# Kernel tuning notes

Hardware: AMD Instinct MI355X
Metric: run time of the kernel (lower is better)

Reference implementation:

```python
import jax, jax.numpy as jnp
import numpy as np

B, N, D = 4, 4096, 256

def setup_inputs() -> dict:
    key = jax.random.key(0)
    ks = jax.random.split(key, 5)
    s = 1.0 / np.sqrt(D)
    return {
        'x': jax.random.normal(ks[0], (B, N, D), jnp.float32),
        'Wq': jax.random.normal(ks[1], (D, D), jnp.float32) * s,
        'bq': jnp.zeros((D,), jnp.float32),
        'Wk': jax.random.normal(ks[2], (D, D), jnp.float32) * s,
        'bk': jnp.zeros((D,), jnp.float32),
        'Wv': jax.random.normal(ks[3], (D, D), jnp.float32) * s,
        'bv': jnp.zeros((D,), jnp.float32),
        'Wfc': jax.random.normal(ks[4], (D, D), jnp.float32) * s,
        'bfc': jnp.zeros((D,), jnp.float32),
    }

def reference(x, Wq, bq, Wk, bk, Wv, bv, Wfc, bfc):
    # Linear layers: y = x @ W^T + b (torch nn.Linear convention)
    q = jnp.einsum('bnd,ed->bne', x, Wq) + bq
    k = jnp.einsum('bnd,ed->bne', x, Wk) + bk
    v = jnp.einsum('bnd,ed->bne', x, Wv) + bv
    # NOTE: source has no 1/sqrt(d) scaling — keep it faithful.
    attn = jnp.einsum('bnd,bmd->bnm', q, k)          # [B, N, N]
    attn = jax.nn.softmax(attn, axis=-1)
    out = jnp.einsum('bnm,bmd->bnd', attn, v)        # [B, N, D]
    out = jnp.einsum('bnd,ed->bne', out, Wfc) + bfc
    return out
```

## Files before the change

kernel.cpp:

```cpp
#include <hip/hip_runtime.h>
#include <stdint.h>

#define B_ 4
#define N_ 4096
#define D_ 256
#define M_ (B_*N_)

typedef _Float16 f16;
typedef _Float16 f16x8 __attribute__((ext_vector_type(8)));
typedef float    f32x4  __attribute__((ext_vector_type(4)));
typedef float    f32x16 __attribute__((ext_vector_type(16)));

#define MFMA16(A,B,C) __builtin_amdgcn_mfma_f32_16x16x32_f16(A,B,C,0,0,0)
#define MFMA32(A,B,C) __builtin_amdgcn_mfma_f32_32x32x16_f16(A,B,C,0,0,0)

#define QH_OFF   0u
#define KH_OFF   8388608u
#define VT_OFF   16777216u
#define WFCH_OFF 25165824u
#define WQS_OFF  25296896u
#define WKS_OFF  25559040u
#define WVS_OFF  25821184u
#define OP_OFF   26083328u
#define ML_OFF   59637760u

typedef __attribute__((address_space(3))) uint32_t lds_u32;
typedef __attribute__((address_space(1))) const uint32_t g_u32;

__device__ __forceinline__ void stage16(const f16* g, f16* lbase) {
    __builtin_amdgcn_global_load_lds((g_u32*)g, (lds_u32*)lbase, 16, 0, 0);
}
__device__ __forceinline__ uint32_t pk2(float a, float b) {
    union { f16 h[2]; uint32_t u; } x;
    x.h[0] = (f16)a; x.h[1] = (f16)b;
    return x.u;
}

__global__ __launch_bounds__(256) void cvt_w(
    const float* __restrict__ Wq, const float* __restrict__ Wk,
    const float* __restrict__ Wv, const float* __restrict__ Wfc,
    f16* __restrict__ Wqs, f16* __restrict__ Wks, f16* __restrict__ Wvs,
    f16* __restrict__ Wfch)
{
    const int z = blockIdx.y;
    const float* W = (z==0) ? Wq : (z==1) ? Wk : (z==2) ? Wv : Wfc;
    int idx = (blockIdx.x * 256 + threadIdx.x) * 4;
    float4 v = *(const float4*)(W + idx);
    union { ushort4 u4; f16 h[4]; } hi, lo;
    float vv[4] = {v.x, v.y, v.z, v.w};
    #pragma unroll
    for (int j = 0; j < 4; j++) {
        hi.h[j] = (f16)vv[j];
        lo.h[j] = (f16)(vv[j] - (float)hi.h[j]);
    }
    int col = idx >> 8, k = idx & 255;
    int dc = k >> 5, c8 = (k >> 3) & 3, j = k & 7;
    int p  = c8 ^ ((col >> 2) & 3);
    if (z == 3) {
        *(ushort4*)(Wfch + dc*8192 + col*32 + p*8 + j) = hi.u4;
    } else {
        f16* Ws = (z==0) ? Wqs : (z==1) ? Wks : Wvs;
        int base = dc*16384 + col*32 + p*8 + j;
        *(ushort4*)(Ws + base)        = hi.u4;
        *(ushort4*)(Ws + base + 8192) = lo.u4;
    }
}

__global__ __launch_bounds__(256, 2) void proj_kernel(
    const float* __restrict__ x,
    const f16* __restrict__ Wqs, const f16* __restrict__ Wks,
    const f16* __restrict__ Wvs,
    const float* __restrict__ bq, const float* __restrict__ bk,
    const float* __restrict__ bv,
    f16* __restrict__ Qh, f16* __restrict__ Kh, f16* __restrict__ Vt)
{
    const int z = blockIdx.y;
    const f16*   Ws   = (z==0) ? Wqs : (z==1) ? Wks : Wvs;
    const float* bias = (z==0) ? bq  : (z==1) ? bk  : bv;

    __shared__ __align__(16) f16 Bs[2][16384];

    const int tid  = threadIdx.x;
    const int w    = tid >> 6;
    const int lane = tid & 63;
    const int l15  = lane & 15;
    const int q4   = lane >> 4;
    const int m0   = blockIdx.x * 64 + w * 16;
    const int rowA = m0 + l15;
    const int sw   = (l15 >> 2) & 3;

    int s8[8];
    #pragma unroll
    for (int i = 0; i < 8; i++) s8[i] = (tid + i*256) * 8;

    f32x4 acc[16];
    #pragma unroll
    for (int nt = 0; nt < 16; nt++) acc[nt] = (f32x4){0.f,0.f,0.f,0.f};

    #pragma unroll
    for (int i = 0; i < 8; i++) stage16(Ws + s8[i], &Bs[0][0] + s8[i]);
    const float* xp = x + (size_t)rowA * 256;
    float4 a0 = *(const float4*)(xp + q4*8);
    float4 a1 = *(const float4*)(xp + q4*8 + 4);

    for (int dc = 0; dc < 8; dc++) {
        const int cur = dc & 1;
        __syncthreads();
        if (dc < 7) {
            const f16* src = Ws + (size_t)(dc+1)*16384;
            f16* dst = &Bs[cur ^ 1][0];
            #pragma unroll
            for (int i = 0; i < 8; i++) stage16(src + s8[i], dst + s8[i]);
        }
        float av[8] = {a0.x,a0.y,a0.z,a0.w,a1.x,a1.y,a1.z,a1.w};
        f16x8 ah, alo;
        #pragma unroll
        for (int j = 0; j < 8; j++) {
            ah[j]  = (f16)av[j];
            alo[j] = (f16)(av[j] - (float)ah[j]);
        }
        if (dc < 7) {
            a0 = *(const float4*)(xp + (dc+1)*32 + q4*8);
            a1 = *(const float4*)(xp + (dc+1)*32 + q4*8 + 4);
        }
        const f16* Bc = &Bs[cur][0];
        #pragma unroll
        for (int nt = 0; nt < 16; nt++) {
            const f16* bp = Bc + (nt*16 + l15)*32 + ((q4 ^ sw) << 3);
            f16x8 bh = *(const f16x8*)bp;
            f16x8 bl = *(const f16x8*)(bp + 8192);
            acc[nt] = MFMA16(ah,  bl, acc[nt]);
            acc[nt] = MFMA16(alo, bh, acc[nt]);
            acc[nt] = MFMA16(ah,  bh, acc[nt]);
        }
    }

    if (z == 0) {
        #pragma unroll
        for (int nt = 0; nt < 16; nt++) {
            float bb = bias[nt*16 + l15];
            #pragma unroll
            for (int r = 0; r < 4; r++)
                Qh[(size_t)(m0 + q4*4 + r)*256 + nt*16 + l15] = (f16)(acc[nt][r] + bb);
        }
    } else if (z == 1) {
        const int cbase = (l15 >> 3);
        const int j     = l15 & 7;
        #pragma unroll
        for (int nt = 0; nt < 16; nt++) {
            float bb = bias[nt*16 + l15];
            int c = nt*2 + cbase;
            #pragma unroll
            for (int r = 0; r < 4; r++) {
                int m = m0 + q4*4 + r;
                Kh[(size_t)m*256 + (size_t)((c ^ (m & 7)) << 3) + j] = (f16)(acc[nt][r] + bb);
            }
        }
    } else {
        uint32_t* VTs = (uint32_t*)&Bs[0][0];
        const int bb_ = m0 >> 12;
        const int n0  = (blockIdx.x * 64) & 4095;
        const int mloc = w*16 + q4*4;
        const int mc   = mloc >> 3;
        __syncthreads();
        #pragma unroll
        for (int nt = 0; nt < 16; nt++) {
            int e = nt*16 + l15;
            float bv_ = bias[e];
            uint32_t w0 = pk2(acc[nt][0]+bv_, acc[nt][1]+bv_);
            uint32_t w1 = pk2(acc[nt][2]+bv_, acc[nt][3]+bv_);
            int base = e*36 + ((mc ^ (e & 7)) << 2) + ((q4*2) & 3);
            VTs[base]     = w0;
            VTs[base + 1] = w1;
        }
        __syncthreads();
        #pragma unroll
        for (int i = 0; i < 8; i++) {
            int e  = w*64 + i*8 + (lane >> 3);
            int nc = lane & 7;
            const f16* src = (const f16*)&VTs[e*36 + ((nc ^ (e & 7)) << 2)];
            f16x8 v = *(const f16x8*)src;
            *(f16x8*)(Vt + ((size_t)bb_*256 + e)*4096 + n0 + nc*8) = v;
        }
    }
}

#define MARGIN 10.0f
__global__ __launch_bounds__(256, 2) void attn_kernel(
    const f16* __restrict__ Qh, const f16* __restrict__ Kh,
    const f16* __restrict__ Vt,
    f16* __restrict__ Opart, float* __restrict__ Ml)
{
    __shared__ __align__(16) f16 SMEM[32768];
    f16* Ks = SMEM;
    f16* Vs = SMEM + 16384;

    const int combo = blockIdx.x & 15;
    const int b   = combo >> 2;
    const int sp  = combo & 3;
    const int qt  = blockIdx.x >> 4;
    const int tid  = threadIdx.x;
    const int w    = tid >> 6;
    const int lane = tid & 63;
    const int l31  = lane & 31;
    const int half = lane >> 5;
    const int qbase = qt * 128 + w * 32;
    const int vx   = (l31 >> 2) & 3;

    f16x8 qf[16];
    {
        const f16* qp = Qh + ((size_t)(b*4096 + qbase + l31))*256 + half*8;
        #pragma unroll
        for (int st = 0; st < 16; st++) qf[st] = *(const f16x8*)(qp + st*16);
    }

    f32x16 Oa[8];
    #pragma unroll
    for (int t = 0; t < 8; t++)
        #pragma unroll
        for (int r = 0; r < 16; r++) Oa[t][r] = 0.f;
    float mo = -3e38f, ls = 0.f;

    const f16* kg0 = Kh + ((size_t)(b*4096 + sp*1024)) * 256;
    const f16* vg0 = Vt + ((size_t)b*256) * 4096 + sp*1024;

    int kslot[4], voff[4];
    #pragma unroll
    for (int i = 0; i < 4; i++) {
        int s = tid + i*256;
        kslot[i] = s * 8;
        int d = s >> 2;
        int kc = (s & 3) ^ ((s >> 4) & 3);
        voff[i] = d * 4096 + kc * 8;
    }

    #pragma unroll
    for (int i = 0; i < 4; i++) stage16(kg0 + kslot[i], Ks + kslot[i]);

    f16x8 bp0, bp1;

    for (int it = 0; it < 32; it++) {
        const int cur = it & 1;
        __syncthreads();
        if (it + 1 < 32) {
            const f16* kg = kg0 + (size_t)(it+1) * 8192;
            f16* kl = Ks + (cur ^ 1) * 8192;
            #pragma unroll
            for (int i = 0; i < 4; i++) stage16(kg + kslot[i], kl + kslot[i]);
        }
        {
            const f16* vg = vg0 + it*32;
            f16* vl = Vs + cur * 8192;
            #pragma unroll
            for (int i = 0; i < 4; i++) stage16(vg + voff[i], vl + kslot[i]);
        }

        const f16* krp = Ks + cur*8192 + l31*256;
        const f16* vpp = Vs + (cur^1)*8192 + l31*32;
        f32x16 sa;
        #pragma unroll
        for (int r = 0; r < 16; r++) sa[r] = 0.f;
        if (it > 0) {
            #pragma unroll
            for (int st = 0; st < 16; st++) {
                f16x8 ka = *(const f16x8*)(krp + (((st*2 + half) ^ (lane & 7)) << 3));
                sa = MFMA32(ka, qf[st], sa);
                int t = st >> 1, kh = st & 1;
                f16x8 va = *(const f16x8*)(vpp + t*1024 + (((half + kh*2) ^ vx) << 3));
                Oa[t] = MFMA32(va, kh ? bp1 : bp0, Oa[t]);
            }
        } else {
            #pragma unroll
            for (int st = 0; st < 16; st++) {
                f16x8 ka = *(const f16x8*)(krp + (((st*2 + half) ^ (lane & 7)) << 3));
                sa = MFMA32(ka, qf[st], sa);
            }
        }

        float tm = sa[0];
        #pragma unroll
        for (int r = 1; r < 16; r++) tm = fmaxf(tm, sa[r]);
        if (__any(tm > mo + MARGIN)) {
            float tmq = fmaxf(tm, __shfl_xor(tm, 32));
            float mn = fmaxf(mo, tmq);
            float al = __expf(mo - mn);
            mo = mn; ls *= al;
            #pragma unroll
            for (int t = 0; t < 8; t++)
                #pragma unroll
                for (int r = 0; r < 16; r++) Oa[t][r] *= al;
        }
        float p[16];
        #pragma unroll
        for (int r = 0; r < 16; r++) { p[r] = __expf(sa[r] - mo); ls += p[r]; }

        #pragma unroll
        for (int kh = 0; kh < 2; kh++) {
            uint32_t lo0 = pk2(p[8*kh+0], p[8*kh+1]);
            uint32_t lo1 = pk2(p[8*kh+2], p[8*kh+3]);
            uint32_t hi0 = pk2(p[8*kh+4], p[8*kh+5]);
            uint32_t hi1 = pk2(p[8*kh+6], p[8*kh+7]);
            uint32_t s0 = half ? lo0 : hi0;
            uint32_t s1 = half ? lo1 : hi1;
            uint32_t r0 = __shfl_xor(s0, 32);
            uint32_t r1 = __shfl_xor(s1, 32);
            uint32_t k0 = half ? hi0 : lo0;
            uint32_t k1 = half ? hi1 : lo1;
            union { uint32_t u[4]; f16x8 v; } bb;
            bb.u[0] = half ? r0 : k0;
            bb.u[1] = half ? r1 : k1;
            bb.u[2] = half ? k0 : r0;
            bb.u[3] = half ? k1 : r1;
            if (kh == 0) bp0 = bb.v; else bp1 = bb.v;
        }
    }

    __syncthreads();
    {
        const f16* vpp = Vs + 8192 + l31*32;
        #pragma unroll
        for (int t = 0; t < 8; t++) {
            #pragma unroll
            for (int kh = 0; kh < 2; kh++) {
                f16x8 va = *(const f16x8*)(vpp + t*1024 + (((half + kh*2) ^ vx) << 3));
                Oa[t] = MFMA32(va, kh ? bp1 : bp0, Oa[t]);
            }
        }
    }
    __syncthreads();

    float l = ls + __shfl_xor(ls, 32);
    float inv = 1.0f / l;
    f16* tb = SMEM + w * 8192;
    #pragma unroll
    for (int t = 0; t < 8; t++) {
        #pragma unroll
        for (int rp = 0; rp < 8; rp++) {
            int r0 = rp * 2;
            int d  = (r0 & 3) + 8*(r0 >> 2) + 4*half + t*32;
            int c  = d >> 3, j = d & 7;
            uint32_t wv = pk2(Oa[t][r0]*inv, Oa[t][r0+1]*inv);
            *(uint32_t*)(tb + l31*256 + ((c ^ (l31 & 7)) << 3) + (j & 6)) = wv;
        }
    }
    f16* opb = Opart + ((size_t)sp*M_ + b*4096 + qbase) * 256;
    #pragma unroll
    for (int i = 0; i < 16; i++) {
        int q = (i & 3)*8 + (lane >> 3);
        int c = (i >> 2)*8 + (lane & 7);
        f16x8 v = *(const f16x8*)(tb + q*256 + ((c ^ (q & 7)) << 3));
        *(f16x8*)(opb + (size_t)q*256 + c*8) = v;
    }
    if (half == 0) {
        size_t mrow = (size_t)sp*M_ + b*4096 + qbase + l31;
        Ml[mrow*2]     = mo;
        Ml[mrow*2 + 1] = l;
    }
}

__global__ __launch_bounds__(256, 2) void merge_fc_kernel(
    const f16* __restrict__ Opart, const float* __restrict__ Ml,
    const f16* __restrict__ Wfci, const float* __restrict__ bfc,
    float* __restrict__ out)
{
    __shared__ __align__(16) f16 Bs[2][8192];

    const int tid  = threadIdx.x;
    const int w    = tid >> 6;
    const int lane = tid & 63;
    const int l15  = lane & 15;
    const int q4   = lane >> 4;
    const int m0   = blockIdx.x * 64 + w * 16;
    const int rowA = m0 + l15;
    const int sw   = (l15 >> 2) & 3;

    int s4[4];
    #pragma unroll
    for (int i = 0; i < 4; i++) s4[i] = (tid + i*256) * 8;

    float mv[4], lv[4];
    #pragma unroll
    for (int p = 0; p < 4; p++) {
        mv[p] = Ml[((size_t)p*M_ + rowA)*2];
        lv[p] = Ml[((size_t)p*M_ + rowA)*2 + 1];
    }
    float mm = fmaxf(fmaxf(mv[0], mv[1]), fmaxf(mv[2], mv[3]));
    float cw[4], den = 0.f;
    #pragma unroll
    for (int p = 0; p < 4; p++) { cw[p] = __expf(mv[p] - mm) * lv[p]; den += cw[p]; }
    float invd = 1.0f / den;
    #pragma unroll
    for (int p = 0; p < 4; p++) cw[p] *= invd;

    #pragma unroll
    for (int i = 0; i < 4; i++) stage16(Wfci + s4[i], &Bs[0][0] + s4[i]);
    const f16* opb = Opart + (size_t)rowA*256 + q4*8;
    f16x8 of[4];
    #pragma unroll
    for (int p = 0; p < 4; p++) of[p] = *(const f16x8*)(opb + (size_t)p*M_*256);

    f32x4 acc[16];
    #pragma unroll
    for (int nt = 0; nt < 16; nt++) acc[nt] = (f32x4){0.f,0.f,0.f,0.f};

    for (int dc = 0; dc < 8; dc++) {
        const int cur = dc & 1;
        __syncthreads();
        if (dc < 7) {
            const f16* src = Wfci + (size_t)(dc+1)*8192;
            f16* dst = &Bs[cur ^ 1][0];
            #pragma unroll
            for (int i = 0; i < 4; i++) stage16(src + s4[i], dst + s4[i]);
        }
        float v[8] = {};
        #pragma unroll
        for (int p = 0; p < 4; p++)
            #pragma unroll
            for (int j = 0; j < 8; j++) v[j] += cw[p] * (float)of[p][j];
        f16x8 af;
        #pragma unroll
        for (int j = 0; j < 8; j++) af[j] = (f16)v[j];
        if (dc < 7) {
            #pragma unroll
            for (int p = 0; p < 4; p++)
                of[p] = *(const f16x8*)(opb + (size_t)p*M_*256 + (dc+1)*32);
        }
        const f16* Bc = &Bs[cur][0];
        #pragma unroll
        for (int nt = 0; nt < 16; nt++) {
            f16x8 bf = *(const f16x8*)(Bc + (nt*16 + l15)*32 + ((q4 ^ sw) << 3));
            acc[nt] = MFMA16(af, bf, acc[nt]);
        }
    }
    #pragma unroll
    for (int nt = 0; nt < 16; nt++) {
        float bias = bfc[nt*16 + l15];
        #pragma unroll
        for (int r = 0; r < 4; r++)
            out[(size_t)(m0 + q4*4 + r) * 256 + nt*16 + l15] = acc[nt][r] + bias;
    }
}

extern "C" void kernel_launch(void* const* d_in, const int* in_sizes, int n_in,
                              void* d_out, int out_size, void* d_ws, size_t ws_size,
                              hipStream_t stream)
{
    const float* x   = (const float*)d_in[0];
    const float* Wq  = (const float*)d_in[1];
    const float* bq  = (const float*)d_in[2];
    const float* Wk  = (const float*)d_in[3];
    const float* bk  = (const float*)d_in[4];
    const float* Wv  = (const float*)d_in[5];
    const float* bv  = (const float*)d_in[6];
    const float* Wfc = (const float*)d_in[7];
    const float* bfc = (const float*)d_in[8];
    float* out = (float*)d_out;

    char* ws = (char*)d_ws;
    f16*   Qh    = (f16*)(ws + QH_OFF);
    f16*   Kh    = (f16*)(ws + KH_OFF);
    f16*   Vt    = (f16*)(ws + VT_OFF);
    f16*   Wfch  = (f16*)(ws + WFCH_OFF);
    f16*   Wqs   = (f16*)(ws + WQS_OFF);
    f16*   Wks   = (f16*)(ws + WKS_OFF);
    f16*   Wvs   = (f16*)(ws + WVS_OFF);
    f16*   Opart = (f16*)(ws + OP_OFF);
    float* Ml    = (float*)(ws + ML_OFF);

    cvt_w<<<dim3(64, 4), 256, 0, stream>>>(Wq, Wk, Wv, Wfc, Wqs, Wks, Wvs, Wfch);
    proj_kernel<<<dim3(256, 3), 256, 0, stream>>>(x, Wqs, Wks, Wvs, bq, bk, bv, Qh, Kh, Vt);
    attn_kernel<<<512, 256, 0, stream>>>(Qh, Kh, Vt, Opart, Ml);
    merge_fc_kernel<<<256, 256, 0, stream>>>(Opart, Ml, Wfch, bfc, out);
}
```

Before: 207.8 us.

## Software-pipeline softmax exp with QK MFMA and fold log2e into Q

Restructures the attention loop into a two-stage pipeline. Each iteration computes the exp of the previous tile's scores while the current tile's QK MFMAs issue, then runs the PV MFMAs. The loop is unrolled by two with templated buffer indices and setprio hints. Q is prescaled by log2(e) so the kernel can use a native exp2 instead of __expf, and the combine step switches to exp2 to match. This adds register pressure from holding two score tiles, and f16 Q now carries the scale factor, which changes rounding slightly.

After: 632.3 us. 3.04x slower.

```diff
diff --git a/kernel.cpp b/kernel.cpp
--- a/kernel.cpp
+++ b/kernel.cpp
@@ -34,6 +34,13 @@
     union { f16 h[2]; uint32_t u; } x;
     x.h[0] = (f16)a; x.h[1] = (f16)b;
     return x.u;
+}
+__device__ __forceinline__ float exp2_fast(float x) {
+#if __has_builtin(__builtin_amdgcn_exp2f)
+    return __builtin_amdgcn_exp2f(x);
+#else
+    return exp2f(x);
+#endif
 }
 
 __global__ __launch_bounds__(256) void cvt_w(
@@ -141,7 +148,8 @@
             float bb = bias[nt*16 + l15];
             #pragma unroll
             for (int r = 0; r < 4; r++)
-                Qh[(size_t)(m0 + q4*4 + r)*256 + nt*16 + l15] = (f16)(acc[nt][r] + bb);
+                Qh[(size_t)(m0 + q4*4 + r)*256 + nt*16 + l15] =
+                    (f16)((acc[nt][r] + bb) * 1.44269504088896f);
         }
     } else if (z == 1) {
         const int cbase = (l15 >> 3);
@@ -185,7 +193,103 @@
     }
 }
 
-#define MARGIN 10.0f
+#define MARGIN2 12.0f
+
+__device__ __forceinline__ void build_bp(const float* p, int half,
+                                         f16x8& bp0, f16x8& bp1)
+{
+    #pragma unroll
+    for (int kh = 0; kh < 2; kh++) {
+        uint32_t lo0 = pk2(p[8*kh+0], p[8*kh+1]);
+        uint32_t lo1 = pk2(p[8*kh+2], p[8*kh+3]);
+        uint32_t hi0 = pk2(p[8*kh+4], p[8*kh+5]);
+        uint32_t hi1 = pk2(p[8*kh+6], p[8*kh+7]);
+        uint32_t s0 = half ? lo0 : hi0;
+        uint32_t s1 = half ? lo1 : hi1;
+        uint32_t r0 = __shfl_xor(s0, 32);
+        uint32_t r1 = __shfl_xor(s1, 32);
+        uint32_t k0 = half ? hi0 : lo0;
+        uint32_t k1 = half ? hi1 : lo1;
+        union { uint32_t u[4]; f16x8 v; } bb;
+        bb.u[0] = half ? r0 : k0;
+        bb.u[1] = half ? r1 : k1;
+        bb.u[2] = half ? k0 : r0;
+        bb.u[3] = half ? k1 : r1;
+        if (kh == 0) bp0 = bb.v; else bp1 = bb.v;
+    }
+}
+
+template<int CUR, bool FIRST, bool LAST>
+__device__ __forceinline__ void attn_body(
+    int it, f32x16& SA, const f32x16& SP, f32x16* Oa, const f16x8* qf,
+    f16x8& bp0, f16x8& bp1, float& mo, float& ls,
+    f16* __restrict__ Ks, f16* __restrict__ Vs,
+    const f16* __restrict__ kg0, const f16* __restrict__ vg0,
+    const int* kslot, const int* voff,
+    int l31, int half, int vx, int lane)
+{
+    __syncthreads();
+    if (!LAST) {
+        const f16* kg = kg0 + (size_t)(it+1) * 8192;
+        f16* kl = Ks + (CUR ^ 1) * 8192;
+        #pragma unroll
+        for (int i = 0; i < 4; i++) stage16(kg + kslot[i], kl + kslot[i]);
+    }
+    {
+        const f16* vg = vg0 + it*32;
+        f16* vl = Vs + CUR * 8192;
+        #pragma unroll
+        for (int i = 0; i < 4; i++) stage16(vg + voff[i], vl + kslot[i]);
+    }
+
+    const f16* krp = Ks + CUR*8192 + l31*256;
+    #pragma unroll
+    for (int r = 0; r < 16; r++) SA[r] = 0.f;
+
+    float p[16];
+    __builtin_amdgcn_s_setprio(1);
+    #pragma unroll
+    for (int st = 0; st < 16; st++) {
+        f16x8 ka = *(const f16x8*)(krp + (((st*2 + half) ^ (lane & 7)) << 3));
+        SA = MFMA32(ka, qf[st], SA);
+        if (!FIRST) p[st] = exp2_fast(SP[st] - mo);
+    }
+    if (!FIRST) {
+        float s0 = (p[0]+p[1]) + (p[2]+p[3]);
+        float s1 = (p[4]+p[5]) + (p[6]+p[7]);
+        float s2 = (p[8]+p[9]) + (p[10]+p[11]);
+        float s3 = (p[12]+p[13]) + (p[14]+p[15]);
+        ls += (s0+s1) + (s2+s3);
+        build_bp(p, half, bp0, bp1);
+        const f16* vpp = Vs + (CUR^1)*8192 + l31*32;
+        #pragma unroll
+        for (int t = 0; t < 8; t++) {
+            #pragma unroll
+            for (int kh = 0; kh < 2; kh++) {
+                f16x8 va = *(const f16x8*)(vpp + t*1024 + (((half + kh*2) ^ vx) << 3));
+                Oa[t] = MFMA32(va, kh ? bp1 : bp0, Oa[t]);
+            }
+        }
+    }
+    __builtin_amdgcn_s_setprio(0);
+
+    float t0 = fmaxf(fmaxf(SA[0],SA[1]),   fmaxf(SA[2],SA[3]));
+    float t1 = fmaxf(fmaxf(SA[4],SA[5]),   fmaxf(SA[6],SA[7]));
+    float t2 = fmaxf(fmaxf(SA[8],SA[9]),   fmaxf(SA[10],SA[11]));
+    float t3 = fmaxf(fmaxf(SA[12],SA[13]), fmaxf(SA[14],SA[15]));
+    float tm = fmaxf(fmaxf(t0,t1), fmaxf(t2,t3));
+    if (__any(tm > mo + MARGIN2)) {
+        float tmq = fmaxf(tm, __shfl_xor(tm, 32));
+        float mn = fmaxf(mo, tmq);
+        float al = exp2_fast(mo - mn);
+        mo = mn; ls *= al;
+        #pragma unroll
+        for (int t = 0; t < 8; t++)
+            #pragma unroll
+            for (int r = 0; r < 16; r++) Oa[t][r] *= al;
+    }
+}
+
 __global__ __launch_bounds__(256, 2) void attn_kernel(
     const f16* __restrict__ Qh, const f16* __restrict__ Kh,
     const f16* __restrict__ Vt,
@@ -238,85 +342,32 @@
     for (int i = 0; i < 4; i++) stage16(kg0 + kslot[i], Ks + kslot[i]);
 
     f16x8 bp0, bp1;
-
-    for (int it = 0; it < 32; it++) {
-        const int cur = it & 1;
-        __syncthreads();
-        if (it + 1 < 32) {
-            const f16* kg = kg0 + (size_t)(it+1) * 8192;
-            f16* kl = Ks + (cur ^ 1) * 8192;
-            #pragma unroll
-            for (int i = 0; i < 4; i++) stage16(kg + kslot[i], kl + kslot[i]);
-        }
-        {
-            const f16* vg = vg0 + it*32;
-            f16* vl = Vs + cur * 8192;
-            #pragma unroll
-            for (int i = 0; i < 4; i++) stage16(vg + voff[i], vl + kslot[i]);
-        }
-
-        const f16* krp = Ks + cur*8192 + l31*256;
-        const f16* vpp = Vs + (cur^1)*8192 + l31*32;
-        f32x16 sa;
-        #pragma unroll
-        for (int r = 0; r < 16; r++) sa[r] = 0.f;
-        if (it > 0) {
-            #pragma unroll
-            for (int st = 0; st < 16; st++) {
-                f16x8 ka = *(const f16x8*)(krp + (((st*2 + half) ^ (lane & 7)) << 3));
-                sa = MFMA32(ka, qf[st], sa);
-                int t = st >> 1, kh = st & 1;
-                f16x8 va = *(const f16x8*)(vpp + t*1024 + (((half + kh*2) ^ vx) << 3));
-                Oa[t] = MFMA32(va, kh ? bp1 : bp0, Oa[t]);
-            }
-        } else {
-            #pragma unroll
-            for (int st = 0; st < 16; st++) {
-                f16x8 ka = *(const f16x8*)(krp + (((st*2 + half) ^ (lane & 7)) << 3));
-                sa = MFMA32(ka, qf[st], sa);
-            }
-        }
-
-        float tm = sa[0];
-        #pragma unroll
-        for (int r = 1; r < 16; r++) tm = fmaxf(tm, sa[r]);
-        if (__any(tm > mo + MARGIN)) {
-            float tmq = fmaxf(tm, __shfl_xor(tm, 32));
-            float mn = fmaxf(mo, tmq);
-            float al = __expf(mo - mn);
-            mo = mn; ls *= al;
-            #pragma unroll
-            for (int t = 0; t < 8; t++)
-                #pragma unroll
-                for (int r = 0; r < 16; r++) Oa[t][r] *= al;
-        }
-        float p[16];
-        #pragma unroll
-        for (int r = 0; r < 16; r++) { p[r] = __expf(sa[r] - mo); ls += p[r]; }
-
-        #pragma unroll
-        for (int kh = 0; kh < 2; kh++) {
-            uint32_t lo0 = pk2(p[8*kh+0], p[8*kh+1]);
-            uint32_t lo1 = pk2(p[8*kh+2], p[8*kh+3]);
-            uint32_t hi0 = pk2(p[8*kh+4], p[8*kh+5]);
-            uint32_t hi1 = pk2(p[8*kh+6], p[8*kh+7]);
-            uint32_t s0 = half ? lo0 : hi0;
-            uint32_t s1 = half ? lo1 : hi1;
-            uint32_t r0 = __shfl_xor(s0, 32);
-            uint32_t r1 = __shfl_xor(s1, 32);
-            uint32_t k0 = half ? hi0 : lo0;
-            uint32_t k1 = half ? hi1 : lo1;
-            union { uint32_t u[4]; f16x8 v; } bb;
-            bb.u[0] = half ? r0 : k0;
-            bb.u[1] = half ? r1 : k1;
-            bb.u[2] = half ? k0 : r0;
-            bb.u[3] = half ? k1 : r1;
-            if (kh == 0) bp0 = bb.v; else bp1 = bb.v;
-        }
-    }
+    f32x16 saA, saB;
+    #pragma unroll
+    for (int r = 0; r < 16; r++) { saA[r] = 0.f; saB[r] = 0.f; }
+
+    attn_body<0, true,  false>(0, saA, saB, Oa, qf, bp0, bp1, mo, ls,
+                               Ks, Vs, kg0, vg0, kslot, voff, l31, half, vx, lane);
+    for (int itp = 0; itp < 15; itp++) {
+        attn_body<1, false, false>(2*itp+1, saB, saA, Oa, qf, bp0, bp1, mo, ls,
+                                   Ks, Vs, kg0, vg0, kslot, voff, l31, half, vx, lane);
+        attn_body<0, false, false>(2*itp+2, saA, saB, Oa, qf, bp0, bp1, mo, ls,
+                                   Ks, Vs, kg0, vg0, kslot, voff, l31, half, vx, lane);
+    }
+    attn_body<1, false, true>(31, saB, saA, Oa, qf, bp0, bp1, mo, ls,
+                              Ks, Vs, kg0, vg0, kslot, voff, l31, half, vx, lane);
 
     __syncthreads();
     {
+        float p[16];
+        #pragma unroll
+        for (int r = 0; r < 16; r++) p[r] = exp2_fast(saB[r] - mo);
+        float s0 = (p[0]+p[1]) + (p[2]+p[3]);
+        float s1 = (p[4]+p[5]) + (p[6]+p[7]);
+        float s2 = (p[8]+p[9]) + (p[10]+p[11]);
+        float s3 = (p[12]+p[13]) + (p[14]+p[15]);
+        ls += (s0+s1) + (s2+s3);
+        build_bp(p, half, bp0, bp1);
         const f16* vpp = Vs + 8192 + l31*32;
         #pragma unroll
         for (int t = 0; t < 8; t++) {
@@ -387,7 +438,7 @@
     float mm = fmaxf(fmaxf(mv[0], mv[1]), fmaxf(mv[2], mv[3]));
     float cw[4], den = 0.f;
     #pragma unroll
-    for (int p = 0; p < 4; p++) { cw[p] = __expf(mv[p] - mm) * lv[p]; den += cw[p]; }
+    for (int p = 0; p < 4; p++) { cw[p] = exp2_fast(mv[p] - mm) * lv[p]; den += cw[p]; }
     float invd = 1.0f / den;
     #pragma unroll
     for (int p = 0; p < 4; p++) cw[p] *= invd;
```

## Halve proj weight staging tiles and split merge_fc output columns across waves

Applied to the files above, without the earlier changes.

The projection kernel now stages the weight in half-width chunks (128 output columns per phase, 16 phases), which halves shared memory per block. The launch bound is raised to allow 3 blocks per CU, and the V transpose epilogue runs in two passes. The merge/FC kernel assigns two waves per 16-row tile, each computing half the output columns, and doubles the grid to 512 blocks to fill more CUs. The cost is more barriers and phases in proj, and merge_fc now re-reads the Opart partials and redoes the softmax-merge weighting twice per row.

After: 211.5 us. Within noise of the previous version (+1.8%).

```diff
diff --git a/kernel.cpp b/kernel.cpp
--- a/kernel.cpp
+++ b/kernel.cpp
@@ -60,13 +60,14 @@
         *(ushort4*)(Wfch + dc*8192 + col*32 + p*8 + j) = hi.u4;
     } else {
         f16* Ws = (z==0) ? Wqs : (z==1) ? Wks : Wvs;
-        int base = dc*16384 + col*32 + p*8 + j;
+        int h  = col >> 7, cl = col & 127;
+        int base = dc*16384 + h*8192 + cl*32 + p*8 + j;
         *(ushort4*)(Ws + base)        = hi.u4;
-        *(ushort4*)(Ws + base + 8192) = lo.u4;
-    }
-}
-
-__global__ __launch_bounds__(256, 2) void proj_kernel(
+        *(ushort4*)(Ws + base + 4096) = lo.u4;
+    }
+}
+
+__global__ __launch_bounds__(256, 3) void proj_kernel(
     const float* __restrict__ x,
     const f16* __restrict__ Wqs, const f16* __restrict__ Wks,
     const f16* __restrict__ Wvs,
@@ -78,7 +79,7 @@
     const f16*   Ws   = (z==0) ? Wqs : (z==1) ? Wks : Wvs;
     const float* bias = (z==0) ? bq  : (z==1) ? bk  : bv;
 
-    __shared__ __align__(16) f16 Bs[2][16384];
+    __shared__ __align__(16) f16 Bs[2][8192];
 
     const int tid  = threadIdx.x;
     const int w    = tid >> 6;
@@ -89,49 +90,53 @@
     const int rowA = m0 + l15;
     const int sw   = (l15 >> 2) & 3;
 
-    int s8[8];
-    #pragma unroll
-    for (int i = 0; i < 8; i++) s8[i] = (tid + i*256) * 8;
+    int s4[4];
+    #pragma unroll
+    for (int i = 0; i < 4; i++) s4[i] = (tid + i*256) * 8;
 
     f32x4 acc[16];
     #pragma unroll
     for (int nt = 0; nt < 16; nt++) acc[nt] = (f32x4){0.f,0.f,0.f,0.f};
 
     #pragma unroll
-    for (int i = 0; i < 8; i++) stage16(Ws + s8[i], &Bs[0][0] + s8[i]);
+    for (int i = 0; i < 4; i++) stage16(Ws + s4[i], &Bs[0][0] + s4[i]);
     const float* xp = x + (size_t)rowA * 256;
     float4 a0 = *(const float4*)(xp + q4*8);
     float4 a1 = *(const float4*)(xp + q4*8 + 4);
-
-    for (int dc = 0; dc < 8; dc++) {
-        const int cur = dc & 1;
+    f16x8 ah, alo;
+
+    for (int ph = 0; ph < 16; ph++) {
+        const int cur = ph & 1;
+        const int dc  = ph >> 1;
+        const int h   = ph & 1;
         __syncthreads();
-        if (dc < 7) {
-            const f16* src = Ws + (size_t)(dc+1)*16384;
+        if (ph < 15) {
+            const f16* src = Ws + (size_t)(ph+1)*8192;
             f16* dst = &Bs[cur ^ 1][0];
             #pragma unroll
-            for (int i = 0; i < 8; i++) stage16(src + s8[i], dst + s8[i]);
-        }
-        float av[8] = {a0.x,a0.y,a0.z,a0.w,a1.x,a1.y,a1.z,a1.w};
-        f16x8 ah, alo;
-        #pragma unroll
-        for (int j = 0; j < 8; j++) {
-            ah[j]  = (f16)av[j];
-            alo[j] = (f16)(av[j] - (float)ah[j]);
-        }
-        if (dc < 7) {
+            for (int i = 0; i < 4; i++) stage16(src + s4[i], dst + s4[i]);
+        }
+        if (h == 0) {
+            float av[8] = {a0.x,a0.y,a0.z,a0.w,a1.x,a1.y,a1.z,a1.w};
+            #pragma unroll
+            for (int j = 0; j < 8; j++) {
+                ah[j]  = (f16)av[j];
+                alo[j] = (f16)(av[j] - (float)ah[j]);
+            }
+        } else if (dc < 7) {
             a0 = *(const float4*)(xp + (dc+1)*32 + q4*8);
             a1 = *(const float4*)(xp + (dc+1)*32 + q4*8 + 4);
         }
         const f16* Bc = &Bs[cur][0];
         #pragma unroll
-        for (int nt = 0; nt < 16; nt++) {
+        for (int nt = 0; nt < 8; nt++) {
             const f16* bp = Bc + (nt*16 + l15)*32 + ((q4 ^ sw) << 3);
             f16x8 bh = *(const f16x8*)bp;
-            f16x8 bl = *(const f16x8*)(bp + 8192);
-            acc[nt] = MFMA16(ah,  bl, acc[nt]);
-            acc[nt] = MFMA16(alo, bh, acc[nt]);
-            acc[nt] = MFMA16(ah,  bh, acc[nt]);
+            f16x8 bl = *(const f16x8*)(bp + 4096);
+            const int ng = h*8 + nt;
+            acc[ng] = MFMA16(ah,  bl, acc[ng]);
+            acc[ng] = MFMA16(alo, bh, acc[ng]);
+            acc[ng] = MFMA16(ah,  bh, acc[ng]);
         }
     }
 
@@ -162,25 +167,30 @@
         const int n0  = (blockIdx.x * 64) & 4095;
         const int mloc = w*16 + q4*4;
         const int mc   = mloc >> 3;
-        __syncthreads();
-        #pragma unroll
-        for (int nt = 0; nt < 16; nt++) {
-            int e = nt*16 + l15;
-            float bv_ = bias[e];
-            uint32_t w0 = pk2(acc[nt][0]+bv_, acc[nt][1]+bv_);
-            uint32_t w1 = pk2(acc[nt][2]+bv_, acc[nt][3]+bv_);
-            int base = e*36 + ((mc ^ (e & 7)) << 2) + ((q4*2) & 3);
-            VTs[base]     = w0;
-            VTs[base + 1] = w1;
-        }
-        __syncthreads();
-        #pragma unroll
-        for (int i = 0; i < 8; i++) {
-            int e  = w*64 + i*8 + (lane >> 3);
-            int nc = lane & 7;
-            const f16* src = (const f16*)&VTs[e*36 + ((nc ^ (e & 7)) << 2)];
-            f16x8 v = *(const f16x8*)src;
-            *(f16x8*)(Vt + ((size_t)bb_*256 + e)*4096 + n0 + nc*8) = v;
+        #pragma unroll
+        for (int P = 0; P < 2; P++) {
+            __syncthreads();
+            #pragma unroll
+            for (int nt = 0; nt < 8; nt++) {
+                int e = P*128 + nt*16 + l15;
+                float bv_ = bias[e];
+                const f32x4& a = acc[P*8 + nt];
+                uint32_t w0 = pk2(a[0]+bv_, a[1]+bv_);
+                uint32_t w1 = pk2(a[2]+bv_, a[3]+bv_);
+                int base = (e & 127)*36 + ((mc ^ (e & 7)) << 2) + ((q4*2) & 3);
+                VTs[base]     = w0;
+                VTs[base + 1] = w1;
+            }
+            __syncthreads();
+            #pragma unroll
+            for (int i = 0; i < 4; i++) {
+                int el = w*32 + i*8 + (lane >> 3);
+                int e  = P*128 + el;
+                int nc = lane & 7;
+                const f16* src = (const f16*)&VTs[el*36 + ((nc ^ (e & 7)) << 2)];
+                f16x8 v = *(const f16x8*)src;
+                *(f16x8*)(Vt + ((size_t)bb_*256 + e)*4096 + n0 + nc*8) = v;
+            }
         }
     }
 }
@@ -370,7 +380,9 @@
     const int lane = tid & 63;
     const int l15  = lane & 15;
     const int q4   = lane >> 4;
-    const int m0   = blockIdx.x * 64 + w * 16;
+    const int rw   = w >> 1;
+    const int nh   = w & 1;
+    const int m0   = blockIdx.x * 32 + rw * 16;
     const int rowA = m0 + l15;
     const int sw   = (l15 >> 2) & 3;
 
@@ -399,9 +411,9 @@
     #pragma unroll
     for (int p = 0; p < 4; p++) of[p] = *(const f16x8*)(opb + (size_t)p*M_*256);
 
-    f32x4 acc[16];
-    #pragma unroll
-    for (int nt = 0; nt < 16; nt++) acc[nt] = (f32x4){0.f,0.f,0.f,0.f};
+    f32x4 acc[8];
+    #pragma unroll
+    for (int nt = 0; nt < 8; nt++) acc[nt] = (f32x4){0.f,0.f,0.f,0.f};
 
     for (int dc = 0; dc < 8; dc++) {
         const int cur = dc & 1;
@@ -427,17 +439,19 @@
         }
         const f16* Bc = &Bs[cur][0];
         #pragma unroll
-        for (int nt = 0; nt < 16; nt++) {
-            f16x8 bf = *(const f16x8*)(Bc + (nt*16 + l15)*32 + ((q4 ^ sw) << 3));
+        for (int nt = 0; nt < 8; nt++) {
+            const int ng = nh*8 + nt;
+            f16x8 bf = *(const f16x8*)(Bc + (ng*16 + l15)*32 + ((q4 ^ sw) << 3));
             acc[nt] = MFMA16(af, bf, acc[nt]);
         }
     }
     #pragma unroll
-    for (int nt = 0; nt < 16; nt++) {
-        float bias = bfc[nt*16 + l15];
+    for (int nt = 0; nt < 8; nt++) {
+        const int ng = nh*8 + nt;
+        float bias = bfc[ng*16 + l15];
         #pragma unroll
         for (int r = 0; r < 4; r++)
-            out[(size_t)(m0 + q4*4 + r) * 256 + nt*16 + l15] = acc[nt][r] + bias;
+            out[(size_t)(m0 + q4*4 + r) * 256 + ng*16 + l15] = acc[nt][r] + bias;
     }
 }
 
@@ -470,5 +484,5 @@
     cvt_w<<<dim3(64, 4), 256, 0, stream>>>(Wq, Wk, Wv, Wfc, Wqs, Wks, Wvs, Wfch);
     proj_kernel<<<dim3(256, 3), 256, 0, stream>>>(x, Wqs, Wks, Wvs, bq, bk, bv, Qh, Kh, Vt);
     attn_kernel<<<512, 256, 0, stream>>>(Qh, Kh, Vt, Opart, Ml);
-    merge_fc_kernel<<<256, 256, 0, stream>>>(Opart, Ml, Wfch, bfc, out);
-}
+    merge_fc_kernel<<<512, 256, 0, stream>>>(Opart, Ml, Wfch, bfc, out);
+}
```
